# Kernel tuning notes

Measured on AMD Instinct MI355X. Metric: run time of the kernel, lower is better.

Reference implementation:

```python
import jax, jax.numpy as jnp
import numpy as np

COST_LABELS = 2.0
COST_BBOX = 5.0
COST_GIOU = 2.0
NUM_HEADS = 7
NUM_CLASSES = 16


def setup_inputs() -> dict:
    key = jax.random.key(0)
    k0, k1, k2, k3 = jax.random.split(key, 4)
    bs, nq, nt = 16, 900, 100
    return {
        "pred_logits": jax.random.normal(k0, (NUM_HEADS, bs, nq, NUM_CLASSES), jnp.float32),
        "pred_boxes": jax.random.uniform(k1, (bs, nq, 4), jnp.float32),
        "tgt_boxes": jax.random.uniform(k2, (bs, nt, 4), jnp.float32),
        "tgt_labels": jax.random.randint(k3, (NUM_HEADS, bs, nt), 0, NUM_CLASSES),
    }


def box_cxcywh_to_xyxy(b):
    cx, cy, w, h = jnp.split(b, 4, axis=-1)
    return jnp.concatenate([cx - 0.5 * w, cy - 0.5 * h, cx + 0.5 * w, cy + 0.5 * h], axis=-1)


def generalized_box_iou(a, b):
    # a: [N,4] xyxy, b: [M,4] xyxy -> [N,M]
    area_a = (a[:, 2] - a[:, 0]) * (a[:, 3] - a[:, 1])
    area_b = (b[:, 2] - b[:, 0]) * (b[:, 3] - b[:, 1])
    lt = jnp.maximum(a[:, None, :2], b[None, :, :2])
    rb = jnp.minimum(a[:, None, 2:], b[None, :, 2:])
    wh = jnp.clip(rb - lt, 0.0)
    inter = wh[..., 0] * wh[..., 1]
    union = area_a[:, None] + area_b[None, :] - inter
    iou = inter / union
    lt_e = jnp.minimum(a[:, None, :2], b[None, :, :2])
    rb_e = jnp.maximum(a[:, None, 2:], b[None, :, 2:])
    wh_e = jnp.clip(rb_e - lt_e, 0.0)
    area = wh_e[..., 0] * wh_e[..., 1]
    return iou - (area - union) / area


@jax.jit
def compute_cost(pred_logits, pred_boxes, tgt_boxes, tgt_labels):
    bs, nq, _ = pred_boxes.shape
    out_bbox = pred_boxes.reshape(-1, 4)   # [N,4] cxcywh
    tgt_bbox = tgt_boxes.reshape(-1, 4)    # [M,4] cxcywh
    # L1 cdist
    cost_bbox = jnp.sum(jnp.abs(out_bbox[:, None, :] - tgt_bbox[None, :, :]), axis=-1)
    cost_giou = -generalized_box_iou(box_cxcywh_to_xyxy(out_bbox), box_cxcywh_to_xyxy(tgt_bbox))
    # label cost: sum over the 7 heads of -sigmoid(logits)[:, tgt_ids]
    probs = jax.nn.sigmoid(pred_logits.reshape(NUM_HEADS, -1, NUM_CLASSES))  # [7,N,C]
    ids = tgt_labels.reshape(NUM_HEADS, -1)                                   # [7,M]
    cost_labels = jnp.zeros_like(cost_bbox)
    for h in range(NUM_HEADS):  # small fixed loop, avoids a [7,N,M] intermediate
        cost_labels = cost_labels - probs[h][:, ids[h]]
    C = COST_BBOX * cost_bbox + COST_LABELS * cost_labels + COST_GIOU * cost_giou
    return C.reshape(bs, nq, -1)  # [bs, nq, bs*nt]


def _lsa(cost):
    """Jonker-Volgenant shortest augmenting path. cost: [r,c] with r<=c.
    Returns row2col: optimal column for each row (minimizes total cost)."""
    cost = np.asarray(cost, dtype=np.float64)
    r, c = cost.shape
    u = np.zeros(r + 1)
    v = np.zeros(c + 1)
    p = np.zeros(c + 1, np.int64)    # p[j] = row matched to column j (1-indexed)
    way = np.zeros(c + 1, np.int64)
    for i in range(1, r + 1):
        p[0] = i
        j0 = 0
        minv = np.full(c + 1, np.inf)
        used = np.zeros(c + 1, bool)
        while True:
            used[j0] = True
            i0 = p[j0]
            free = np.nonzero(~used)[0]  # unused columns (1..c)
            cur = cost[i0 - 1, free - 1] - u[i0] - v[free]
            better = cur < minv[free]
            minv[free] = np.where(better, cur, minv[free])
            way[free[better]] = j0
            k = np.argmin(minv[free])
            j1 = free[k]
            delta = minv[free][k]
            u[p[used]] += delta
            v[used] -= delta
            minv[free] -= delta
            j0 = j1
            if p[j0] == 0:
                break
        while j0:
            j1 = way[j0]
            p[j0] = p[j1]
            j0 = j1
    row2col = np.full(r, -1, np.int64)
    for j in range(1, c + 1):
        if p[j] > 0:
            row2col[p[j] - 1] = j - 1
    return row2col


def reference(pred_logits, pred_boxes, tgt_boxes, tgt_labels):
    C = compute_cost(pred_logits, pred_boxes, tgt_boxes, tgt_labels)  # [bs, nq, bs*nt]
    bs, nq, M = C.shape
    nt = M // bs
    Cn = np.asarray(C)
    out = np.zeros((bs, 2, nt), np.int64)
    for b in range(bs):
        sub = Cn[b, :, b * nt:(b + 1) * nt]  # [nq, nt] per-image block (mimics C.split(sizes))
        t2p = _lsa(sub.T)                    # for each target, its matched prediction
        order = np.argsort(t2p, kind="stable")  # scipy returns row indices sorted
        out[b, 0] = t2p[order]  # index_i: selected predictions (sorted)
        out[b, 1] = order       # index_j: corresponding targets
    return jnp.asarray(out)
```

## Files before the change

kernel.cpp:

```cpp
#include <hip/hip_runtime.h>
#include <hip/hip_bf16.h>
#include <math.h>

#define NQ 900
#define NT 100
#define BS 16
#define NH 7
#define NC 16
#define NSLOT 16
#define MAXTREE 8192

__global__ __launch_bounds__(256) void cost_kernel(const float*  __restrict__ logits,
                                                   const float4* __restrict__ pboxes4,
                                                   const float4* __restrict__ tboxes4,
                                                   const int*    __restrict__ tlabels,
                                                   float* __restrict__ costT) {
    const int bt = blockIdx.x;
    const int b = bt / NT, t = bt % NT;

    int lab[NH];
    #pragma unroll
    for (int h = 0; h < NH; ++h) lab[h] = tlabels[(h * BS + b) * NT + t];

    float4 tb = tboxes4[b * NT + t];
    float tx = tb.x, ty = tb.y, tw = tb.z, th = tb.w;
    float bx0 = tx - 0.5f * tw, by0 = ty - 0.5f * th;
    float bx1 = tx + 0.5f * tw, by1 = ty + 0.5f * th;
    float areaB = (bx1 - bx0) * (by1 - by0);

    for (int q = threadIdx.x; q < NQ; q += 256) {
        float4 pb = pboxes4[b * NQ + q];
        float px = pb.x, py = pb.y, pw = pb.z, ph = pb.w;

        float cost_bbox = fabsf(px - tx) + fabsf(py - ty) + fabsf(pw - tw) + fabsf(ph - th);

        float ax0 = px - 0.5f * pw, ay0 = py - 0.5f * ph;
        float ax1 = px + 0.5f * pw, ay1 = py + 0.5f * ph;
        float areaA = (ax1 - ax0) * (ay1 - ay0);
        float ltx = fmaxf(ax0, bx0), lty = fmaxf(ay0, by0);
        float rbx = fminf(ax1, bx1), rby = fminf(ay1, by1);
        float iw = fmaxf(rbx - ltx, 0.f), ih = fmaxf(rby - lty, 0.f);
        float inter = iw * ih;
        float uni = areaA + areaB - inter;
        float iou = inter / uni;
        float ex0 = fminf(ax0, bx0), ey0 = fminf(ay0, by0);
        float ex1 = fmaxf(ax1, bx1), ey1 = fmaxf(ay1, by1);
        float ew = fmaxf(ex1 - ex0, 0.f), eh = fmaxf(ey1 - ey0, 0.f);
        float earea = ew * eh;
        float giou = iou - (earea - uni) / earea;

        float ssum = 0.f;
        #pragma unroll
        for (int h = 0; h < NH; ++h) {
            float x = logits[(size_t)((h * BS + b) * NQ + q) * NC + lab[h]];
            ssum += 1.0f / (1.0f + expf(-x));
        }

        costT[(b * NT + t) * NQ + q] = 5.0f * cost_bbox - 2.0f * ssum - 2.0f * giou;
    }
}

__global__ __launch_bounds__(64) void lsa_kernel(const float* __restrict__ costT,
                                                 int* __restrict__ out) {
    const int b = blockIdx.x;
    const int lane = threadIdx.x;
    const float* cost = costT + b * NT * NQ;

    __shared__ float u_s[NT + 1];
    __shared__ int p_s[NQ + 1];
    __shared__ int way2[NSLOT][64];
    __shared__ int p_w[NQ + 1];
    __shared__ int jmin_s[NT];
    __shared__ int listA[NT];
    __shared__ int r2c[NT];
    __shared__ int cnt_s;

    for (int j = lane; j <= NQ; j += 64) {
        p_s[j] = 0;
        p_w[j] = 0x7fffffff;
    }
    __syncthreads();

    bool lostA = false, lostB = false;
    #pragma unroll
    for (int pass = 0; pass < 2; ++pass) {
        int r = pass * 64 + lane;
        if (r < NT) {
            const float4* row4 = (const float4*)(cost + (size_t)r * NQ);
            float m0 = INFINITY, m1f = INFINITY, m2f = INFINITY, m3f = INFINITY;
            int i0 = 0, i1 = 0, i2 = 0, i3 = 0;
            #pragma unroll 5
            for (int q4 = 0; q4 < NQ / 4; ++q4) {
                float4 cv = row4[q4];
                if (cv.x < m0)  { m0 = cv.x;  i0 = 4 * q4; }
                if (cv.y < m1f) { m1f = cv.y; i1 = 4 * q4 + 1; }
                if (cv.z < m2f) { m2f = cv.z; i2 = 4 * q4 + 2; }
                if (cv.w < m3f) { m3f = cv.w; i3 = 4 * q4 + 3; }
            }
            float mv = m0; int mj = i0;
            if (m1f < mv || (m1f == mv && i1 < mj)) { mv = m1f; mj = i1; }
            if (m2f < mv || (m2f == mv && i2 < mj)) { mv = m2f; mj = i2; }
            if (m3f < mv || (m3f == mv && i3 < mj)) { mv = m3f; mj = i3; }
            u_s[r + 1] = mv;
            jmin_s[r] = mj;
            atomicMin(&p_w[mj + 1], r + 1);
        }
    }
    __syncthreads();

    {
        int rA = lane;
        int j = jmin_s[rA] + 1;
        if (p_w[j] == rA + 1) p_s[j] = rA + 1;
        else lostA = true;
    }
    if (lane < NT - 64) {
        int rB = 64 + lane;
        int j = jmin_s[rB] + 1;
        if (p_w[j] == rB + 1) p_s[j] = rB + 1;
        else lostB = true;
    }
    unsigned long long mA = __ballot(lostA);
    unsigned long long mB = __ballot(lostB);
    if (lane == 0) {
        int n = 0;
        unsigned long long m = mA;
        while (m) { int l = __ffsll((unsigned long long)m) - 1; listA[n++] = l + 1; m &= m - 1; }
        m = mB;
        while (m) { int l = __ffsll((unsigned long long)m) - 1; listA[n++] = 64 + l + 1; m &= m - 1; }
        cnt_s = n;
    }
    __syncthreads();
    const int nfree = cnt_s;

    float v[NSLOT], minv[NSLOT], upreg[NSLOT], dreg[NSLOT], biasreg[NSLOT];
    int preg[NSLOT], wayreg[NSLOT];
    int jof[NSLOT];
    const unsigned invalid = (lane <= 32) ? 0u : 0xF000u;
    #pragma unroll
    for (int s = 0; s < NSLOT; ++s) {
        v[s] = 0.0f; dreg[s] = 0.0f; wayreg[s] = 0;
        biasreg[s] = ((invalid >> s) & 1u) ? INFINITY : 0.0f;
        jof[s] = 1 + 4 * lane + 256 * (s >> 2) + (s & 3);
        int pr = 0;
        if (!((invalid >> s) & 1u)) pr = p_s[jof[s]];
        preg[s] = pr;
        upreg[s] = (pr > 0) ? u_s[pr] : 0.0f;
    }
    __syncthreads();

    for (int ii = 0; ii < nfree; ++ii) {
        const int i = listA[ii];
        #pragma unroll
        for (int s = 0; s < NSLOT; ++s) minv[s] = INFINITY;
        unsigned used = invalid;
        int j0 = 0;
        int i0 = i;
        float u_i0 = u_s[i];
        const float u_root = u_i0;
        float d0 = 0.0f;
        float deltaf = 0.0f;
        int guard = 0;

        while (guard++ < MAXTREE) {
            if (j0 != 0) {
                int idx = j0 - 1;
                if (lane == ((idx >> 2) & 63)) {
                    int slot = ((idx >> 8) << 2) | (idx & 3);
                    used |= (1u << slot);
                    #pragma unroll
                    for (int s = 0; s < NSLOT; ++s)
                        if (s == slot) { dreg[s] = d0; minv[s] = INFINITY; biasreg[s] = INFINITY; }
                }
            }

            const float4* crow4 = (const float4*)(cost + (size_t)(i0 - 1) * NQ);
            float4 c4[4];
            #pragma unroll
            for (int kc = 0; kc < 3; ++kc) c4[kc] = crow4[lane + 64 * kc];
            c4[3] = (lane <= 32) ? crow4[lane + 192] : make_float4(0.f, 0.f, 0.f, 0.f);

            const float duv = d0 - u_i0;
            #pragma unroll
            for (int kc = 0; kc < 4; ++kc) {
                #pragma unroll
                for (int e = 0; e < 4; ++e) {
                    const int s = 4 * kc + e;
                    float cf = (e == 0) ? c4[kc].x : (e == 1) ? c4[kc].y
                             : (e == 2) ? c4[kc].z : c4[kc].w;
                    float cand = ((cf + biasreg[s]) + duv) - v[s];
                    bool imp = cand < minv[s];
                    minv[s] = imp ? cand : minv[s];
                    wayreg[s] = imp ? j0 : wayreg[s];
                }
            }

            float tm[NSLOT]; int tj[NSLOT];
            #pragma unroll
            for (int s = 0; s < NSLOT; ++s) { tm[s] = minv[s]; tj[s] = jof[s]; }
            #pragma unroll
            for (int st = 8; st >= 1; st >>= 1) {
                #pragma unroll
                for (int s = 0; s < 8; ++s) {
                    if (s < st) {
                        if (tm[s + st] < tm[s]) { tm[s] = tm[s + st]; tj[s] = tj[s + st]; }
                    }
                }
            }
            const float bv = tm[0];
            const int bj = tj[0];

            float vmin = bv;
            #pragma unroll
            for (int off = 1; off < 64; off <<= 1)
                vmin = fminf(vmin, __shfl_xor(vmin, off));
            unsigned long long tied = __ballot(bv == vmin);
            int wl = __ffsll((unsigned long long)tied) - 1;
            int jwin = __shfl(bj, wl);

            int bs = (((bj - 1) >> 8) << 2) | ((bj - 1) & 3);
            int pb = 0; float ub2 = 0.0f;
            #pragma unroll
            for (int s = 0; s < NSLOT; ++s)
                if (s == bs) { pb = preg[s]; ub2 = upreg[s]; }
            int i0n = __shfl(pb, wl);
            float u_n = __shfl(ub2, wl);

            j0 = jwin;
            d0 = vmin;
            if (i0n == 0) { deltaf = vmin; break; }
            i0 = i0n;
            u_i0 = u_n;
        }

        #pragma unroll
        for (int s = 0; s < NSLOT; ++s) way2[s][lane] = wayreg[s];
        #pragma unroll
        for (int s = 0; s < NSLOT; ++s) {
            if (((used >> s) & 1u) && !((invalid >> s) & 1u)) {
                v[s] += (dreg[s] - deltaf);
                u_s[preg[s]] = upreg[s] + (deltaf - dreg[s]);
                biasreg[s] = 0.0f;
            }
        }
        if (lane == 0) u_s[i] = u_root + deltaf;
        __syncthreads();
        if (lane == 0) {
            int j = j0;
            while (j) {
                int idx = j - 1;
                int ol = (idx >> 2) & 63;
                int sl = ((idx >> 8) << 2) | (idx & 3);
                int jw = way2[sl][ol];
                p_s[j] = (jw == 0) ? i : p_s[jw];
                j = jw;
            }
        }
        __syncthreads();
        #pragma unroll
        for (int s = 0; s < NSLOT; ++s) {
            if (!((invalid >> s) & 1u)) {
                if (((used >> s) & 1u) || (jof[s] == j0)) {
                    int pr = p_s[jof[s]];
                    preg[s] = pr;
                    upreg[s] = (pr > 0) ? u_s[pr] : 0.0f;
                }
            }
        }
    }

    __syncthreads();
    for (int j = 1 + lane; j <= NQ; j += 64) {
        int pi = p_s[j];
        if (pi > 0) r2c[pi - 1] = j - 1;
    }
    __syncthreads();
    for (int t = lane; t < NT; t += 64) {
        int ccol = r2c[t];
        int rank = 0;
        for (int tt = 0; tt < NT; ++tt) rank += (r2c[tt] < ccol) ? 1 : 0;
        out[b * 2 * NT + rank] = ccol;
        out[b * 2 * NT + NT + rank] = t;
    }
}

extern "C" void kernel_launch(void* const* d_in, const int* in_sizes, int n_in,
                              void* d_out, int out_size, void* d_ws, size_t ws_size,
                              hipStream_t stream) {
    const float* logits  = (const float*)d_in[0];
    const float* pboxes  = (const float*)d_in[1];
    const float* tboxes  = (const float*)d_in[2];
    const int*   tlabels = (const int*)d_in[3];
    int* out = (int*)d_out;
    float* costT = (float*)d_ws;

    cost_kernel<<<BS * NT, 256, 0, stream>>>(logits, (const float4*)pboxes,
                                             (const float4*)tboxes, tlabels, costT);
    lsa_kernel<<<BS, 64, 0, stream>>>(costT, out);
}
```

Before: 104.0 us.

## Precompute transposed sigmoid probs and prefetch next cost row in LSA loop

Adds a kernel that applies the sigmoid to the logits once and stores them transposed (class-major) in workspace. The cost kernel then reads the needed per-label probabilities as coalesced rows instead of recomputing the sigmoid from strided logits for every target. Separately, the LSA inner loop now issues the next cost-row load right after the next row index is known, and prefetches the first row of the following free row early, to hide global-load latency on the serial augmenting path. Costs are one extra launch, extra workspace, and higher register pressure.

```diff
diff --git a/kernel.cpp b/kernel.cpp
--- a/kernel.cpp
+++ b/kernel.cpp
@@ -10,11 +10,78 @@
 #define NSLOT 16
 #define MAXTREE 8192
 
-__global__ __launch_bounds__(256) void cost_kernel(const float*  __restrict__ logits,
-                                                   const float4* __restrict__ pboxes4,
-                                                   const float4* __restrict__ tboxes4,
-                                                   const int*    __restrict__ tlabels,
-                                                   float* __restrict__ costT) {
+__global__ __launch_bounds__(256) void sig_transpose_kernel(const float* __restrict__ logits,
+                                                            float* __restrict__ probsT) {
+    const int hb = blockIdx.x;
+    const float* src = logits + (size_t)hb * NQ * NC;
+    float* dst = probsT + (size_t)hb * NC * NQ;
+    __shared__ float tile[NC][NQ + 1];
+    for (int e = threadIdx.x; e < NQ * NC; e += 256) {
+        int q = e >> 4, c = e & 15;
+        float x = src[e];
+        tile[c][q] = 1.0f / (1.0f + expf(-x));
+    }
+    __syncthreads();
+    for (int c = 0; c < NC; ++c)
+        for (int q = threadIdx.x; q < NQ; q += 256)
+            dst[c * NQ + q] = tile[c][q];
+}
+
+__global__ __launch_bounds__(256) void cost_kernel_bt(const float4* __restrict__ pboxes4,
+                                                      const float4* __restrict__ tboxes4,
+                                                      const int*    __restrict__ tlabels,
+                                                      const float*  __restrict__ probsT,
+                                                      float* __restrict__ costT) {
+    const int bt = blockIdx.x;
+    const int b = bt / NT, t = bt % NT;
+
+    const float* prow[NH];
+    #pragma unroll
+    for (int h = 0; h < NH; ++h) {
+        int lab = tlabels[(h * BS + b) * NT + t];
+        prow[h] = probsT + (size_t)((h * BS + b) * NC + lab) * NQ;
+    }
+
+    float4 tb = tboxes4[b * NT + t];
+    float tx = tb.x, ty = tb.y, tw = tb.z, th = tb.w;
+    float bx0 = tx - 0.5f * tw, by0 = ty - 0.5f * th;
+    float bx1 = tx + 0.5f * tw, by1 = ty + 0.5f * th;
+    float areaB = (bx1 - bx0) * (by1 - by0);
+
+    for (int q = threadIdx.x; q < NQ; q += 256) {
+        float4 pb = pboxes4[b * NQ + q];
+        float px = pb.x, py = pb.y, pw = pb.z, ph = pb.w;
+
+        float cost_bbox = fabsf(px - tx) + fabsf(py - ty) + fabsf(pw - tw) + fabsf(ph - th);
+
+        float ax0 = px - 0.5f * pw, ay0 = py - 0.5f * ph;
+        float ax1 = px + 0.5f * pw, ay1 = py + 0.5f * ph;
+        float areaA = (ax1 - ax0) * (ay1 - ay0);
+        float ltx = fmaxf(ax0, bx0), lty = fmaxf(ay0, by0);
+        float rbx = fminf(ax1, bx1), rby = fminf(ay1, by1);
+        float iw = fmaxf(rbx - ltx, 0.f), ih = fmaxf(rby - lty, 0.f);
+        float inter = iw * ih;
+        float uni = areaA + areaB - inter;
+        float iou = inter / uni;
+        float ex0 = fminf(ax0, bx0), ey0 = fminf(ay0, by0);
+        float ex1 = fmaxf(ax1, bx1), ey1 = fmaxf(ay1, by1);
+        float ew = fmaxf(ex1 - ex0, 0.f), eh = fmaxf(ey1 - ey0, 0.f);
+        float earea = ew * eh;
+        float giou = iou - (earea - uni) / earea;
+
+        float ssum = 0.f;
+        #pragma unroll
+        for (int h = 0; h < NH; ++h) ssum += prow[h][q];
+
+        costT[(b * NT + t) * NQ + q] = 5.0f * cost_bbox - 2.0f * ssum - 2.0f * giou;
+    }
+}
+
+__global__ __launch_bounds__(256) void cost_kernel_fb(const float*  __restrict__ logits,
+                                                      const float4* __restrict__ pboxes4,
+                                                      const float4* __restrict__ tboxes4,
+                                                      const int*    __restrict__ tlabels,
+                                                      float* __restrict__ costT) {
     const int bt = blockIdx.x;
     const int b = bt / NT, t = bt % NT;
 
@@ -149,6 +216,14 @@
     }
     __syncthreads();
 
+    float4 c4pre[4];
+    if (nfree > 0) {
+        const float4* r4 = (const float4*)(cost + (size_t)(listA[0] - 1) * NQ);
+        #pragma unroll
+        for (int kc = 0; kc < 3; ++kc) c4pre[kc] = r4[lane + 64 * kc];
+        c4pre[3] = (lane <= 32) ? r4[lane + 192] : make_float4(0.f, 0.f, 0.f, 0.f);
+    }
+
     for (int ii = 0; ii < nfree; ++ii) {
         const int i = listA[ii];
         #pragma unroll
@@ -161,6 +236,10 @@
         float d0 = 0.0f;
         float deltaf = 0.0f;
         int guard = 0;
+
+        float4 c4[4];
+        #pragma unroll
+        for (int kc = 0; kc < 4; ++kc) c4[kc] = c4pre[kc];
 
         while (guard++ < MAXTREE) {
             if (j0 != 0) {
@@ -173,12 +252,6 @@
                         if (s == slot) { dreg[s] = d0; minv[s] = INFINITY; biasreg[s] = INFINITY; }
                 }
             }
-
-            const float4* crow4 = (const float4*)(cost + (size_t)(i0 - 1) * NQ);
-            float4 c4[4];
-            #pragma unroll
-            for (int kc = 0; kc < 3; ++kc) c4[kc] = crow4[lane + 64 * kc];
-            c4[3] = (lane <= 32) ? crow4[lane + 192] : make_float4(0.f, 0.f, 0.f, 0.f);
 
             const float duv = d0 - u_i0;
             #pragma unroll
@@ -231,6 +304,18 @@
             if (i0n == 0) { deltaf = vmin; break; }
             i0 = i0n;
             u_i0 = u_n;
+
+            const float4* crow4 = (const float4*)(cost + (size_t)(i0 - 1) * NQ);
+            #pragma unroll
+            for (int kc = 0; kc < 3; ++kc) c4[kc] = crow4[lane + 64 * kc];
+            c4[3] = (lane <= 32) ? crow4[lane + 192] : make_float4(0.f, 0.f, 0.f, 0.f);
+        }
+
+        if (ii + 1 < nfree) {
+            const float4* r4 = (const float4*)(cost + (size_t)(listA[ii + 1] - 1) * NQ);
+            #pragma unroll
+            for (int kc = 0; kc < 3; ++kc) c4pre[kc] = r4[lane + 64 * kc];
+            c4pre[3] = (lane <= 32) ? r4[lane + 192] : make_float4(0.f, 0.f, 0.f, 0.f);
         }
 
         #pragma unroll
@@ -294,7 +379,18 @@
     int* out = (int*)d_out;
     float* costT = (float*)d_ws;
 
-    cost_kernel<<<BS * NT, 256, 0, stream>>>(logits, (const float4*)pboxes,
-                                             (const float4*)tboxes, tlabels, costT);
+    const size_t costT_elems  = (size_t)BS * NT * NQ;
+    const size_t probsT_elems = (size_t)NH * BS * NC * NQ;
+    const size_t need = (costT_elems + probsT_elems) * sizeof(float);
+
+    if (ws_size >= need) {
+        float* probsT = costT + costT_elems;
+        sig_transpose_kernel<<<NH * BS, 256, 0, stream>>>(logits, probsT);
+        cost_kernel_bt<<<BS * NT, 256, 0, stream>>>((const float4*)pboxes,
+                                                    (const float4*)tboxes, tlabels, probsT, costT);
+    } else {
+        cost_kernel_fb<<<BS * NT, 256, 0, stream>>>(logits, (const float4*)pboxes,
+                                                    (const float4*)tboxes, tlabels, costT);
+    }
     lsa_kernel<<<BS, 64, 0, stream>>>(costT, out);
 }
```

After: 103.3 us, median of 2. Within noise of the previous version (-0.7%).
